# Performance work log

Hardware: AMD Instinct MI355X
Metric: run time of the kernel (lower is better)

Reference implementation:

```python
import jax, jax.numpy as jnp
import numpy as np
from jax import lax

B, C, L, N = 64, 64, 8192, 3
F = L // 2 + 1  # rfft bins = 4097
HID = 2 * C     # CnnEncoder ratio=2 -> 128
K = 3           # conv kernel size


def setup_inputs() -> dict:
    key = jax.random.key(0)
    ks = jax.random.split(key, 10)
    inp = {
        "x": jax.random.normal(ks[0], (B, C, L), dtype=jnp.float32),
        # spectral filter bank: [N, C, F, 2] (real/imag stacked)
        "parameter": jax.random.normal(ks[1], (N, C, F, 2), dtype=jnp.float32),
        # reweight_R CnnEncoder params (PyTorch Conv1d layout: [out, in, k])
        "wR1": jax.random.normal(ks[2], (HID, C, K), dtype=jnp.float32) * 0.05,
        "bR1": jnp.zeros((HID,), dtype=jnp.float32),
        "wR2": jax.random.normal(ks[3], (N, HID, K), dtype=jnp.float32) * 0.05,
        "bR2": jnp.zeros((N,), dtype=jnp.float32),
        # reweight_I CnnEncoder params
        "wI1": jax.random.normal(ks[4], (HID, C, K), dtype=jnp.float32) * 0.05,
        "bI1": jnp.zeros((HID,), dtype=jnp.float32),
        "wI2": jax.random.normal(ks[5], (N, HID, K), dtype=jnp.float32) * 0.05,
        "bI2": jnp.zeros((N,), dtype=jnp.float32),
    }
    return inp


def _conv1d_same(x, w, b):
    # x: [B, Cin, L]; w: [Cout, Cin, K]; SAME padding for odd K
    pad = (w.shape[-1] - 1) // 2
    y = lax.conv_general_dilated(
        x, w, window_strides=(1,), padding=[(pad, pad)],
        dimension_numbers=("NCH", "OIH", "NCH"))
    return y + b[None, :, None]


def _cnn_encoder(x, w1, b1, w2, b2):
    # conv -> SELU -> (dropout=identity in eval) -> conv -> global avg pool -> softmax over channels
    y = jax.nn.selu(_conv1d_same(x, w1, b1))
    y = _conv1d_same(y, w2, b2)
    y = jnp.mean(y, axis=-1)          # AdaptiveAvgPool1d(1) + squeeze -> [B, N]
    return jax.nn.softmax(y, axis=1)


def reference(x, parameter, wR1, bR1, wR2, bR2, wI1, bI1, wI2, bI2):
    fx = jnp.fft.rfft(x, axis=-1, norm="ortho")          # [B, C, F] complex
    W_R = parameter[..., 0]                               # [N, C, F]
    W_I = parameter[..., 1]
    C_R = _cnn_encoder(fx.real, wR1, bR1, wR2, bR2)       # [B, N]
    C_I = _cnn_encoder(fx.imag, wI1, bI1, wI2, bI2)       # [B, N]
    Kf_R = jnp.einsum("bn,ncf->bcf", C_R, W_R)            # [B, C, F]
    Kf_I = jnp.einsum("bn,ncf->bcf", C_I, W_I)
    Kf = lax.complex(Kf_R, Kf_I)
    out = jnp.fft.irfft(fx * Kf, n=L, axis=-1, norm="ortho")  # [B, C, L]
    return out
```

## Files before the change

### kernel.cpp

```cpp
#include <hip/hip_runtime.h>
#include <math.h>

#define BB 64
#define CCH 64
#define LL 8192
#define FF 4097
#define FP 4104
#define M4 4096
#define NT 65

typedef __attribute__((ext_vector_type(8))) short short8;
typedef __attribute__((ext_vector_type(4))) float floatx4;

__device__ __forceinline__ short f2bf(float v) {
    union { float f; unsigned u; } cv; cv.f = v;
    unsigned r = (cv.u + 0x7fffu + ((cv.u >> 16) & 1u)) >> 16;
    return (short)r;
}

__device__ __forceinline__ float2 cadd(float2 a, float2 b){ return make_float2(a.x+b.x, a.y+b.y); }
__device__ __forceinline__ float2 csub(float2 a, float2 b){ return make_float2(a.x-b.x, a.y-b.y); }
__device__ __forceinline__ float2 cmul(float2 a, float2 b){ return make_float2(a.x*b.x-a.y*b.y, a.x*b.y+a.y*b.x); }
template<int SIGN> __device__ __forceinline__ float2 roti(float2 a){
    return (SIGN < 0) ? make_float2(a.y, -a.x) : make_float2(-a.y, a.x);
}
template<int SIGN>
__device__ __forceinline__ void dft4(float2& a, float2& b, float2& c, float2& d){
    float2 t0 = cadd(a,c), t1 = csub(a,c), t2 = cadd(b,d), t3 = roti<SIGN>(csub(b,d));
    a = cadd(t0,t2); b = cadd(t1,t3); c = csub(t0,t2); d = csub(t1,t3);
}

template<int SIGN>
__device__ __forceinline__ void dft16(float2 v[16]){
    const float C1 = 0.9238795325112867f, S1 = 0.3826834323650898f, R2 = 0.7071067811865476f;
    const float sg = (SIGN < 0) ? -1.0f : 1.0f;
#pragma unroll
    for (int n1 = 0; n1 < 4; ++n1) dft4<SIGN>(v[n1], v[n1+4], v[n1+8], v[n1+12]);
    const float2 W1 = make_float2( C1, sg*S1);
    const float2 W2 = make_float2( R2, sg*R2);
    const float2 W3 = make_float2( S1, sg*C1);
    const float2 W6 = make_float2(-R2, sg*R2);
    const float2 W9 = make_float2(-C1, -sg*S1);
    v[5]  = cmul(v[5],  W1); v[6]  = cmul(v[6],  W2); v[7]  = cmul(v[7],  W3);
    v[9]  = cmul(v[9],  W2); v[10] = roti<SIGN>(v[10]); v[11] = cmul(v[11], W6);
    v[13] = cmul(v[13], W3); v[14] = cmul(v[14], W6); v[15] = cmul(v[15], W9);
#pragma unroll
    for (int k2 = 0; k2 < 4; ++k2) dft4<SIGN>(v[4*k2+0], v[4*k2+1], v[4*k2+2], v[4*k2+3]);
    float2 t[16];
#pragma unroll
    for (int k = 0; k < 16; ++k) t[k] = v[4*(k & 3) + (k >> 2)];
#pragma unroll
    for (int k = 0; k < 16; ++k) v[k] = t[k];
}

__device__ __forceinline__ void twiddle_pow(float2 v[16], float ang){
    float s, c; __sincosf(ang, &s, &c);
    float2 w = make_float2(c, s), t = w;
    v[1] = cmul(v[1], t);
#pragma unroll
    for (int j = 2; j < 16; ++j){ t = cmul(t, w); v[j] = cmul(v[j], t); }
}

template<int SIGN>
__device__ __forceinline__ void fft4096_regs(float2 v[16], float2* lds, int tid){
    const float TWO_PI = 6.283185307179586f;
    const float sg = (SIGN < 0) ? -1.0f : 1.0f;
    int n1 = tid & 15, hi = tid >> 4;
    dft16<SIGN>(v);
    twiddle_pow(v, sg * TWO_PI * (float)hi * (1.0f/256.0f));
#pragma unroll
    for (int j = 0; j < 16; ++j) lds[tid + 272*j] = v[j];
    __syncthreads();
#pragma unroll
    for (int j = 0; j < 16; ++j) v[j] = lds[n1 + 16*j + 272*hi];
    __syncthreads();
    dft16<SIGN>(v);
#pragma unroll
    for (int j = 0; j < 16; ++j) lds[(j*16 + hi)*17 + n1] = v[j];
    __syncthreads();
#pragma unroll
    for (int j = 0; j < 16; ++j) v[j] = lds[tid*17 + j];
    twiddle_pow(v, sg * TWO_PI * (float)tid * (1.0f/4096.0f));
    dft16<SIGN>(v);
    __syncthreads();
}

#define COSJ_INIT { 1.0f, 0.980785280403230f, 0.923879532511287f, 0.831469612302545f, \
    0.707106781186548f, 0.555570233019602f, 0.382683432365090f, 0.195090322016128f, \
    0.0f, -0.195090322016128f, -0.382683432365090f, -0.555570233019602f, \
    -0.707106781186548f, -0.831469612302545f, -0.923879532511287f, -0.980785280403230f }
#define SINJ_INIT { 0.0f, 0.195090322016128f, 0.382683432365090f, 0.555570233019602f, \
    0.707106781186548f, 0.831469612302545f, 0.923879532511287f, 0.980785280403230f, \
    1.0f, 0.980785280403230f, 0.923879532511287f, 0.831469612302545f, \
    0.707106781186548f, 0.555570233019602f, 0.382683432365090f, 0.195090322016128f }

__global__ __launch_bounds__(256, 4) void k_rfft(const float* __restrict__ x,
                                                 float* __restrict__ fxr,
                                                 float* __restrict__ fxi)
{
    __shared__ float2 lds[4352];
    int bc = blockIdx.x, tid = threadIdx.x;
    const float2* xr = (const float2*)(x + (size_t)bc * LL);
    float2 v[16];
#pragma unroll
    for (int j = 0; j < 16; ++j) v[j] = xr[tid + 256*j];
    fft4096_regs<-1>(v, lds, tid);
#pragma unroll
    for (int j = 0; j < 16; ++j) lds[tid + 256*j] = v[j];
    __syncthreads();

    const float scale = 0.011048543456039806f;
    const float COSJ[16] = COSJ_INIT;
    const float SINJ[16] = SINJ_INIT;
    size_t row = (size_t)bc * FP;
    float sA, cA; __sincosf(3.14159265358979f * (float)tid * (1.0f/4096.0f), &sA, &cA);
#pragma unroll
    for (int j = 0; j < 16; ++j){
        int k = tid + 256*j;
        if (k == 0){
            float2 z0 = lds[0];
            fxr[row + 0]  = (z0.x + z0.y) * scale; fxi[row + 0]  = 0.0f;
            fxr[row + M4] = (z0.x - z0.y) * scale; fxi[row + M4] = 0.0f;
        } else {
            float2 zk = lds[k], zm = lds[(4096 - k) & 4095];
            float er = 0.5f*(zk.x + zm.x), ei = 0.5f*(zk.y - zm.y);
            float dr = 0.5f*(zk.x - zm.x), di = 0.5f*(zk.y + zm.y);
            float cp = cA*COSJ[j] - sA*SINJ[j];
            float sp = sA*COSJ[j] + cA*SINJ[j];
            fxr[row + k] = (er + cp*di - sp*dr) * scale;
            fxi[row + k] = (ei - cp*dr - sp*di) * scale;
        }
    }
}

__global__ __launch_bounds__(256) void k_pack(const float* __restrict__ wR1,
                                              const float* __restrict__ wI1,
                                              short* __restrict__ Wp)
{
    int idx = blockIdx.x * 256 + threadIdx.x;
    if (idx >= 2 * 128 * 192) return;
    int enc = idx / (128 * 192);
    int rem = idx - enc * (128 * 192);
    int h = rem / 192;
    int k = rem - h * 192;
    int s = k >> 5;
    int j = k & 31;
    int kap = s >> 1;
    int c = (s & 1) * 32 + j;
    const float* w = enc ? wI1 : wR1;
    Wp[idx] = f2bf(w[(h * 64 + c) * 3 + kap]);
}

__global__ __launch_bounds__(256, 5) void k_conv_mfma(const float* __restrict__ fxr,
                                                      const float* __restrict__ fxi,
                                                      const short* __restrict__ Wp,
                                                      const float* __restrict__ bR1,
                                                      const float* __restrict__ bI1,
                                                      float* __restrict__ part,
                                                      float* __restrict__ e0,
                                                      float* __restrict__ e1)
{
    __shared__ short Xt[66 * 64];
    int tile = blockIdx.x;
    int b    = blockIdx.y;
    int enc  = blockIdx.z;
    const float* src = enc ? fxi : fxr;
    const float* b1  = enc ? bI1 : bR1;
    int tid = threadIdx.x;
    int t0 = tile * 64;
    const float* xb = src + (size_t)b * 64 * FP;

    int w = tid >> 6;
    int lane = tid & 63;
    int n = lane & 15;
    int q = lane >> 4;
    int h0 = w * 32;

    short8 afrag[2][6];
    const short* wbase = Wp + (size_t)enc * 128 * 192;
#pragma unroll
    for (int hb = 0; hb < 2; ++hb)
#pragma unroll
        for (int s = 0; s < 6; ++s)
            afrag[hb][s] = *(const short8*)(wbase + (h0 + hb * 16 + n) * 192 + s * 32 + q * 8);

    float4 b1q[2];
#pragma unroll
    for (int hb = 0; hb < 2; ++hb)
        b1q[hb] = *(const float4*)(b1 + h0 + hb * 16 + q * 4);

    int sw  = tid >> 6;
    int scc = tid & 63;
    {
        const float* srow = xb + (size_t)scc * FP + t0 + sw * 16;
        float4 f0 = *(const float4*)(srow + 0);
        float4 f1 = *(const float4*)(srow + 4);
        float4 f2 = *(const float4*)(srow + 8);
        float4 f3 = *(const float4*)(srow + 12);
        float vals[16] = { f0.x, f0.y, f0.z, f0.w,  f1.x, f1.y, f1.z, f1.w,
                           f2.x, f2.y, f2.z, f2.w,  f3.x, f3.y, f3.z, f3.w };
        bool allv = (t0 + 64) <= FF;
#pragma unroll
        for (int u = 0; u < 16; ++u) {
            float val = vals[u];
            if (!allv) val = (t0 + sw * 16 + u) < FF ? val : 0.0f;
            int tt = sw * 16 + u + 1;
            Xt[(tt * 64 + scc) ^ ((tt & 7) << 3)] = f2bf(val);
        }
        if (tid < 128) {
            int hhal = tid >> 6;
            int ht = hhal ? (t0 + 64) : (t0 - 1);
            int hts = ht < 0 ? 0 : (ht >= FF ? FF - 1 : ht);
            float v = xb[(size_t)scc * FP + hts];
            if (ht < 0 || ht >= FF) v = 0.0f;
            int tt = hhal ? 65 : 0;
            Xt[(tt * 64 + scc) ^ ((tt & 7) << 3)] = f2bf(v);
        }
    }

#pragma unroll
    for (int hb = 0; hb < 2; ++hb)
#pragma unroll
        for (int s = 0; s < 6; ++s)
            asm volatile("" :: "v"(afrag[hb][s]));

    __syncthreads();

    floatx4 acc[2][4];
#pragma unroll
    for (int hb = 0; hb < 2; ++hb)
#pragma unroll
        for (int tb = 0; tb < 4; ++tb) {
            acc[hb][tb][0] = b1q[hb].x;
            acc[hb][tb][1] = b1q[hb].y;
            acc[hb][tb][2] = b1q[hb].z;
            acc[hb][tb][3] = b1q[hb].w;
        }

#pragma unroll
    for (int s = 0; s < 6; ++s) {
        int kap = s >> 1;
        int cbase = (s & 1) * 32 + q * 8;
#pragma unroll
        for (int tb = 0; tb < 4; ++tb) {
            int row = tb * 16 + n + kap;
            short8 bfrag = *(const short8*)(Xt + ((row * 64 + cbase) ^ ((row & 7) << 3)));
            acc[0][tb] = __builtin_amdgcn_mfma_f32_16x16x32_bf16(afrag[0][s], bfrag, acc[0][tb], 0, 0, 0);
            acc[1][tb] = __builtin_amdgcn_mfma_f32_16x16x32_bf16(afrag[1][s], bfrag, acc[1][tb], 0, 0, 0);
        }
    }

    const float SELU_S = 1.0507009873554805f;
    const float SELU_A = 1.6732632423543772f;
    int ebase = (enc * 64 + b) * 128;
    bool edge = (t0 == 0) || (t0 == 4096);
    bool allv = (t0 + 63) < FF;
    float hsum[2][4] = {{0.f,0.f,0.f,0.f},{0.f,0.f,0.f,0.f}};
#pragma unroll
    for (int hb = 0; hb < 2; ++hb) {
#pragma unroll
        for (int tb = 0; tb < 4; ++tb) {
            int t = t0 + tb * 16 + n;
            bool valid = t < FF;
#pragma unroll
            for (int r = 0; r < 4; ++r) {
                float val = acc[hb][tb][r];
                float y = SELU_S * (val > 0.0f ? val : SELU_A * (__expf(val) - 1.0f));
                if (!allv) y = valid ? y : 0.0f;
                hsum[hb][r] += y;
                if (edge) {
                    int h = h0 + hb * 16 + q * 4 + r;
                    if (t == 0)      e0[ebase + h] = y;
                    if (t == FF - 1) e1[ebase + h] = y;
                }
            }
        }
    }

#pragma unroll
    for (int off = 1; off < 16; off <<= 1)
#pragma unroll
        for (int hb = 0; hb < 2; ++hb)
#pragma unroll
            for (int r = 0; r < 4; ++r)
                hsum[hb][r] += __shfl_xor(hsum[hb][r], off, 64);

    if (n == 0) {
#pragma unroll
        for (int hb = 0; hb < 2; ++hb) {
            size_t idx = ((size_t)(tile * 2 + enc) * 64 + b) * 128 + h0 + hb * 16 + q * 4;
            *(float4*)(part + idx) = make_float4(hsum[hb][0], hsum[hb][1], hsum[hb][2], hsum[hb][3]);
        }
    }
}

__global__ __launch_bounds__(128) void k_head(const float* __restrict__ part,
                                              const float* __restrict__ e0,
                                              const float* __restrict__ e1,
                                              const float* __restrict__ wR2,
                                              const float* __restrict__ bR2,
                                              const float* __restrict__ wI2,
                                              const float* __restrict__ bI2,
                                              float* __restrict__ Cw)
{
    __shared__ float red[3][128];
    int b   = blockIdx.x;
    int enc = blockIdx.y;
    const float* w2 = enc ? wI2 : wR2;
    const float* b2 = enc ? bI2 : bR2;
    int h = threadIdx.x;
    float T = 0.0f;
    for (int t = 0; t < NT; ++t)
        T += part[((size_t)(t * 2 + enc) * 64 + b) * 128 + h];
    float e0v = e0[(enc * 64 + b) * 128 + h];
    float e1v = e1[(enc * 64 + b) * 128 + h];
#pragma unroll
    for (int nn = 0; nn < 3; ++nn) {
        const float* wp = w2 + (nn * 128 + h) * 3;
        red[nn][h] = wp[0] * (T - e1v) + wp[1] * T + wp[2] * (T - e0v);
    }
    __syncthreads();
    if (h < 64) {
        float lg[3];
#pragma unroll
        for (int nn = 0; nn < 3; ++nn) {
            float s = red[nn][h] + red[nn][h + 64];
#pragma unroll
            for (int off = 1; off < 64; off <<= 1)
                s += __shfl_xor(s, off, 64);
            lg[nn] = b2[nn] + s / 4097.0f;
        }
        if (h == 0) {
            float mx = fmaxf(lg[0], fmaxf(lg[1], lg[2]));
            float ex0 = __expf(lg[0] - mx);
            float ex1 = __expf(lg[1] - mx);
            float ex2 = __expf(lg[2] - mx);
            float den = ex0 + ex1 + ex2;
            Cw[(enc * 64 + b) * 3 + 0] = ex0 / den;
            Cw[(enc * 64 + b) * 3 + 1] = ex1 / den;
            Cw[(enc * 64 + b) * 3 + 2] = ex2 / den;
        }
    }
}

__global__ __launch_bounds__(256, 4) void k_irfft(const float* __restrict__ fxr,
                                                  const float* __restrict__ fxi,
                                                  const float* __restrict__ param,
                                                  const float* __restrict__ Cw,
                                                  float* __restrict__ out)
{
    __shared__ float2 lds[4352];
    int bc = blockIdx.x, b = bc >> 6, c = bc & 63, tid = threadIdx.x;
    float cr0 = Cw[b*3+0], cr1 = Cw[b*3+1], cr2 = Cw[b*3+2];
    float ci0 = Cw[192 + b*3+0], ci1 = Cw[192 + b*3+1], ci2 = Cw[192 + b*3+2];
    size_t row = (size_t)bc * FP;
    const float2* W0 = (const float2*)param + (size_t)(0*64 + c) * FF;
    const float2* W1 = (const float2*)param + (size_t)(1*64 + c) * FF;
    const float2* W2 = (const float2*)param + (size_t)(2*64 + c) * FF;

    for (int f = tid; f <= 4096; f += 256) {
        float2 w0 = W0[f], w1 = W1[f], w2 = W2[f];
        float kr = cr0*w0.x + cr1*w1.x + cr2*w2.x;
        float ki = ci0*w0.y + ci1*w1.y + ci2*w2.y;
        float fr = fxr[row + f], fi = fxi[row + f];
        lds[f] = make_float2(fr*kr - fi*ki, fr*ki + fi*kr);
    }
    __syncthreads();

    const float COSJ[16] = COSJ_INIT;
    const float SINJ[16] = SINJ_INIT;
    float2 v[16];
    float sA, cA; __sincosf(3.14159265358979f * (float)tid * (1.0f/4096.0f), &sA, &cA);
#pragma unroll
    for (int j = 0; j < 16; ++j) {
        int m = tid + 256*j;
        if (m == 0) {
            float p0 = lds[0].x, pn = lds[4096].x;
            v[j] = make_float2(0.5f*(p0 + pn), 0.5f*(p0 - pn));
        } else {
            float2 p = lds[m], qq = lds[4096 - m];
            float er = 0.5f*(p.x + qq.x), ei = 0.5f*(p.y - qq.y);
            float dr = 0.5f*(p.x - qq.x), di = 0.5f*(p.y + qq.y);
            float cp = cA*COSJ[j] - sA*SINJ[j];
            float sp = sA*COSJ[j] + cA*SINJ[j];
            float zor = dr*cp - di*sp;
            float zoi = dr*sp + di*cp;
            v[j] = make_float2(er - zoi, ei + zor);
        }
    }
    __syncthreads();
    fft4096_regs<1>(v, lds, tid);

    const float S = 0.02209708691207961f;
    float2* orow = (float2*)(out + (size_t)bc * LL);
#pragma unroll
    for (int j = 0; j < 16; ++j) {
        float2 z = v[j];
        orow[tid + 256*j] = make_float2(S*z.x, S*z.y);
    }
}

extern "C" void kernel_launch(void* const* d_in, const int* in_sizes, int n_in,
                              void* d_out, int out_size, void* d_ws, size_t ws_size,
                              hipStream_t stream)
{
    (void)in_sizes; (void)n_in; (void)out_size; (void)ws_size;
    const float* x   = (const float*)d_in[0];
    const float* prm = (const float*)d_in[1];
    const float* wR1 = (const float*)d_in[2];
    const float* bR1 = (const float*)d_in[3];
    const float* wR2 = (const float*)d_in[4];
    const float* bR2 = (const float*)d_in[5];
    const float* wI1 = (const float*)d_in[6];
    const float* bI1 = (const float*)d_in[7];
    const float* wI2 = (const float*)d_in[8];
    const float* bI2 = (const float*)d_in[9];
    float* out = (float*)d_out;
    float* ws  = (float*)d_ws;

    size_t o = 0;
    float* fxr  = ws + o; o += (size_t)BB * CCH * FP;
    float* fxi  = ws + o; o += (size_t)BB * CCH * FP;
    float* part = ws + o; o += (size_t)NT * 2 * 64 * 128;
    float* e0   = ws + o; o += 2 * 64 * 128;
    float* e1   = ws + o; o += 2 * 64 * 128;
    float* Cw   = ws + o; o += 2 * 64 * 4;
    short* Wp   = (short*)(ws + o); o += (size_t)2 * 128 * 192 / 2;

    k_rfft<<<dim3(4096), dim3(256), 0, stream>>>(x, fxr, fxi);
    k_pack<<<dim3((2 * 128 * 192 + 255) / 256), dim3(256), 0, stream>>>(wR1, wI1, Wp);
    k_conv_mfma<<<dim3(NT, 64, 2), dim3(256), 0, stream>>>(fxr, fxi, Wp, bR1, bI1,
                                                           part, e0, e1);
    k_head<<<dim3(64, 2), dim3(128), 0, stream>>>(part, e0, e1, wR2, bR2, wI2, bI2, Cw);
    k_irfft<<<dim3(4096), dim3(256), 0, stream>>>(fxr, fxi, prm, Cw, out);
}
```

Measured before the change: 380.9 us.

## Interleave spectrum as complex float2 and shrink FFT LDS with XOR swizzle

Stores the rfft output as one interleaved float2 array instead of separate real and imaginary planes, so rfft and irfft issue single 8-byte accesses. The conv kernel now reads twice the bytes and keeps only the half it needs. The FFT transposes drop the padded 272/17-stride LDS layout for an XOR swizzle, and irfft packs the Nyquist bin into lds[0].y. Together these cut LDS to 32KB so rfft and irfft can run 5 blocks per CU instead of 4. The trade-off is extra conv read traffic and a possibly imperfect bank-conflict pattern from the swizzle.

```diff
diff --git a/kernel.cpp b/kernel.cpp
--- a/kernel.cpp
+++ b/kernel.cpp
@@ -69,17 +69,17 @@
     dft16<SIGN>(v);
     twiddle_pow(v, sg * TWO_PI * (float)hi * (1.0f/256.0f));
 #pragma unroll
-    for (int j = 0; j < 16; ++j) lds[tid + 272*j] = v[j];
-    __syncthreads();
-#pragma unroll
-    for (int j = 0; j < 16; ++j) v[j] = lds[n1 + 16*j + 272*hi];
+    for (int j = 0; j < 16; ++j) lds[j*256 + tid] = v[j];
+    __syncthreads();
+#pragma unroll
+    for (int j = 0; j < 16; ++j) v[j] = lds[hi*256 + j*16 + n1];
     __syncthreads();
     dft16<SIGN>(v);
 #pragma unroll
-    for (int j = 0; j < 16; ++j) lds[(j*16 + hi)*17 + n1] = v[j];
-    __syncthreads();
-#pragma unroll
-    for (int j = 0; j < 16; ++j) v[j] = lds[tid*17 + j];
+    for (int j = 0; j < 16; ++j) lds[(j*16 + hi)*16 + (n1 ^ hi)] = v[j];
+    __syncthreads();
+#pragma unroll
+    for (int j = 0; j < 16; ++j) v[j] = lds[tid*16 + (j ^ n1)];
     twiddle_pow(v, sg * TWO_PI * (float)tid * (1.0f/4096.0f));
     dft16<SIGN>(v);
     __syncthreads();
@@ -94,11 +94,10 @@
     1.0f, 0.980785280403230f, 0.923879532511287f, 0.831469612302545f, \
     0.707106781186548f, 0.555570233019602f, 0.382683432365090f, 0.195090322016128f }
 
-__global__ __launch_bounds__(256, 4) void k_rfft(const float* __restrict__ x,
-                                                 float* __restrict__ fxr,
-                                                 float* __restrict__ fxi)
-{
-    __shared__ float2 lds[4352];
+__global__ __launch_bounds__(256, 5) void k_rfft(const float* __restrict__ x,
+                                                 float2* __restrict__ fxc)
+{
+    __shared__ float2 lds[4096];
     int bc = blockIdx.x, tid = threadIdx.x;
     const float2* xr = (const float2*)(x + (size_t)bc * LL);
     float2 v[16];
@@ -112,23 +111,23 @@
     const float scale = 0.011048543456039806f;
     const float COSJ[16] = COSJ_INIT;
     const float SINJ[16] = SINJ_INIT;
-    size_t row = (size_t)bc * FP;
+    float2* fc = fxc + (size_t)bc * FP;
     float sA, cA; __sincosf(3.14159265358979f * (float)tid * (1.0f/4096.0f), &sA, &cA);
 #pragma unroll
     for (int j = 0; j < 16; ++j){
         int k = tid + 256*j;
         if (k == 0){
             float2 z0 = lds[0];
-            fxr[row + 0]  = (z0.x + z0.y) * scale; fxi[row + 0]  = 0.0f;
-            fxr[row + M4] = (z0.x - z0.y) * scale; fxi[row + M4] = 0.0f;
+            fc[0]  = make_float2((z0.x + z0.y) * scale, 0.0f);
+            fc[M4] = make_float2((z0.x - z0.y) * scale, 0.0f);
         } else {
             float2 zk = lds[k], zm = lds[(4096 - k) & 4095];
             float er = 0.5f*(zk.x + zm.x), ei = 0.5f*(zk.y - zm.y);
             float dr = 0.5f*(zk.x - zm.x), di = 0.5f*(zk.y + zm.y);
             float cp = cA*COSJ[j] - sA*SINJ[j];
             float sp = sA*COSJ[j] + cA*SINJ[j];
-            fxr[row + k] = (er + cp*di - sp*dr) * scale;
-            fxi[row + k] = (ei - cp*dr - sp*di) * scale;
+            fc[k] = make_float2((er + cp*di - sp*dr) * scale,
+                                (ei - cp*dr - sp*di) * scale);
         }
     }
 }
@@ -151,8 +150,7 @@
     Wp[idx] = f2bf(w[(h * 64 + c) * 3 + kap]);
 }
 
-__global__ __launch_bounds__(256, 5) void k_conv_mfma(const float* __restrict__ fxr,
-                                                      const float* __restrict__ fxi,
+__global__ __launch_bounds__(256, 5) void k_conv_mfma(const float2* __restrict__ fxc,
                                                       const short* __restrict__ Wp,
                                                       const float* __restrict__ bR1,
                                                       const float* __restrict__ bI1,
@@ -164,11 +162,10 @@
     int tile = blockIdx.x;
     int b    = blockIdx.y;
     int enc  = blockIdx.z;
-    const float* src = enc ? fxi : fxr;
     const float* b1  = enc ? bI1 : bR1;
     int tid = threadIdx.x;
     int t0 = tile * 64;
-    const float* xb = src + (size_t)b * 64 * FP;
+    const float2* xb = fxc + (size_t)b * 64 * FP;
 
     int w = tid >> 6;
     int lane = tid & 63;
@@ -192,13 +189,16 @@
     int sw  = tid >> 6;
     int scc = tid & 63;
     {
-        const float* srow = xb + (size_t)scc * FP + t0 + sw * 16;
-        float4 f0 = *(const float4*)(srow + 0);
-        float4 f1 = *(const float4*)(srow + 4);
-        float4 f2 = *(const float4*)(srow + 8);
-        float4 f3 = *(const float4*)(srow + 12);
-        float vals[16] = { f0.x, f0.y, f0.z, f0.w,  f1.x, f1.y, f1.z, f1.w,
-                           f2.x, f2.y, f2.z, f2.w,  f3.x, f3.y, f3.z, f3.w };
+        const float4* srow4 = (const float4*)(xb + (size_t)scc * FP + t0 + sw * 16);
+        float4 g[8];
+#pragma unroll
+        for (int i = 0; i < 8; ++i) g[i] = srow4[i];
+        float vals[16];
+#pragma unroll
+        for (int i = 0; i < 8; ++i) {
+            vals[2*i]   = enc ? g[i].y : g[i].x;
+            vals[2*i+1] = enc ? g[i].w : g[i].z;
+        }
         bool allv = (t0 + 64) <= FF;
 #pragma unroll
         for (int u = 0; u < 16; ++u) {
@@ -211,7 +211,8 @@
             int hhal = tid >> 6;
             int ht = hhal ? (t0 + 64) : (t0 - 1);
             int hts = ht < 0 ? 0 : (ht >= FF ? FF - 1 : ht);
-            float v = xb[(size_t)scc * FP + hts];
+            float2 hp = xb[(size_t)scc * FP + hts];
+            float v = enc ? hp.y : hp.x;
             if (ht < 0 || ht >= FF) v = 0.0f;
             int tt = hhal ? 65 : 0;
             Xt[(tt * 64 + scc) ^ ((tt & 7) << 3)] = f2bf(v);
@@ -343,27 +344,33 @@
     }
 }
 
-__global__ __launch_bounds__(256, 4) void k_irfft(const float* __restrict__ fxr,
-                                                  const float* __restrict__ fxi,
+__global__ __launch_bounds__(256, 5) void k_irfft(const float2* __restrict__ fxc,
                                                   const float* __restrict__ param,
                                                   const float* __restrict__ Cw,
                                                   float* __restrict__ out)
 {
-    __shared__ float2 lds[4352];
+    __shared__ float2 lds[4096];
     int bc = blockIdx.x, b = bc >> 6, c = bc & 63, tid = threadIdx.x;
     float cr0 = Cw[b*3+0], cr1 = Cw[b*3+1], cr2 = Cw[b*3+2];
     float ci0 = Cw[192 + b*3+0], ci1 = Cw[192 + b*3+1], ci2 = Cw[192 + b*3+2];
-    size_t row = (size_t)bc * FP;
+    const float2* fc = fxc + (size_t)bc * FP;
     const float2* W0 = (const float2*)param + (size_t)(0*64 + c) * FF;
     const float2* W1 = (const float2*)param + (size_t)(1*64 + c) * FF;
     const float2* W2 = (const float2*)param + (size_t)(2*64 + c) * FF;
 
-    for (int f = tid; f <= 4096; f += 256) {
+    for (int f = tid; f < 4096; f += 256) {
         float2 w0 = W0[f], w1 = W1[f], w2 = W2[f];
         float kr = cr0*w0.x + cr1*w1.x + cr2*w2.x;
         float ki = ci0*w0.y + ci1*w1.y + ci2*w2.y;
-        float fr = fxr[row + f], fi = fxi[row + f];
-        lds[f] = make_float2(fr*kr - fi*ki, fr*ki + fi*kr);
+        float2 fx = fc[f];
+        float Pr = fx.x*kr - fx.y*ki;
+        float Pi = fx.x*ki + fx.y*kr;
+        if (f == 0) {
+            float2 u0 = W0[4096], u1 = W1[4096], u2 = W2[4096];
+            float krn = cr0*u0.x + cr1*u1.x + cr2*u2.x;
+            Pi = fc[4096].x * krn;
+        }
+        lds[f] = make_float2(Pr, Pi);
     }
     __syncthreads();
 
@@ -375,7 +382,7 @@
     for (int j = 0; j < 16; ++j) {
         int m = tid + 256*j;
         if (m == 0) {
-            float p0 = lds[0].x, pn = lds[4096].x;
+            float p0 = lds[0].x, pn = lds[0].y;
             v[j] = make_float2(0.5f*(p0 + pn), 0.5f*(p0 - pn));
         } else {
             float2 p = lds[m], qq = lds[4096 - m];
@@ -419,18 +426,17 @@
     float* ws  = (float*)d_ws;
 
     size_t o = 0;
-    float* fxr  = ws + o; o += (size_t)BB * CCH * FP;
-    float* fxi  = ws + o; o += (size_t)BB * CCH * FP;
+    float2* fxc = (float2*)(ws + o); o += (size_t)BB * CCH * FP * 2;
     float* part = ws + o; o += (size_t)NT * 2 * 64 * 128;
     float* e0   = ws + o; o += 2 * 64 * 128;
     float* e1   = ws + o; o += 2 * 64 * 128;
     float* Cw   = ws + o; o += 2 * 64 * 4;
     short* Wp   = (short*)(ws + o); o += (size_t)2 * 128 * 192 / 2;
 
-    k_rfft<<<dim3(4096), dim3(256), 0, stream>>>(x, fxr, fxi);
+    k_rfft<<<dim3(4096), dim3(256), 0, stream>>>(x, fxc);
     k_pack<<<dim3((2 * 128 * 192 + 255) / 256), dim3(256), 0, stream>>>(wR1, wI1, Wp);
-    k_conv_mfma<<<dim3(NT, 64, 2), dim3(256), 0, stream>>>(fxr, fxi, Wp, bR1, bI1,
+    k_conv_mfma<<<dim3(NT, 64, 2), dim3(256), 0, stream>>>(fxc, Wp, bR1, bI1,
                                                            part, e0, e1);
     k_head<<<dim3(64, 2), dim3(128), 0, stream>>>(part, e0, e1, wR2, bR2, wI2, bI2, Cw);
-    k_irfft<<<dim3(4096), dim3(256), 0, stream>>>(fxr, fxi, prm, Cw, out);
-}
+    k_irfft<<<dim3(4096), dim3(256), 0, stream>>>(fxc, prm, Cw, out);
+}
```

After: 405.5 us. +6.5%, slower.
